# Kernel tuning notes

Measured on AMD Instinct MI355X. Metric: run time of the kernel, lower is better.

The kernel has to match this reference:

```python
import jax, jax.numpy as jnp
import numpy as np

N = 64      # features
L = 96      # history length
LP = 24     # prediction length
H = 128     # rnn hidden
B = 1024    # batch


def setup_inputs() -> dict:
    key = jax.random.key(0)
    ks = jax.random.split(key, 16)
    # monotonically increasing timestamps
    tp_all = jnp.cumsum(jax.random.uniform(ks[0], (B, L + LP), dtype=jnp.float32), axis=1)
    tp_true = tp_all[:, :L]
    tp_pred = tp_all[:, L:]
    X = jax.random.normal(ks[1], (B, L, N), dtype=jnp.float32)
    mask = jax.random.randint(ks[2], (B, L, N), 0, 2).astype(jnp.float32)
    def unif(k, shape, fan):
        std = 1.0 / np.sqrt(fan)
        return jax.random.uniform(k, shape, jnp.float32, -std, std)
    # TemporalDecay for h: W (H,N), b (H); std = 1/sqrt(out)
    Wh_dec = unif(ks[3], (H, N), H)
    bh_dec = unif(ks[4], (H,), H)
    # TemporalDecay for x (diag): W (N,N) but only diagonal used
    Wx_dec = unif(ks[5], (N, N), N)
    bx_dec = unif(ks[6], (N,), N)
    # GRUCell: input size = 2N + H
    in_sz = 2 * N + H
    W_ih = unif(ks[7], (3 * H, in_sz), H)
    W_hh = unif(ks[8], (3 * H, H), H)
    b_ih = unif(ks[9], (3 * H,), H)
    b_hh = unif(ks[10], (3 * H,), H)
    # output projection
    Wp = unif(ks[11], (N, H), H)
    bp = unif(ks[12], (N,), H)
    return {"tp_pred": tp_pred, "X": X, "tp_true": tp_true, "mask": mask,
            "Wh_dec": Wh_dec, "bh_dec": bh_dec, "Wx_dec": Wx_dec, "bx_dec": bx_dec,
            "W_ih": W_ih, "W_hh": W_hh, "b_ih": b_ih, "b_hh": b_hh,
            "Wp": Wp, "bp": bp}


def _grud(tp_pred, X, tp_true, mask, Wh_dec, bh_dec, Wx_dec, bx_dec,
          W_ih, W_hh, b_ih, b_hh, Wp, bp):
    Bsz, Lh, Nf = X.shape
    Lp = tp_pred.shape[1]
    Lall = Lh + Lp
    Hh = Wh_dec.shape[0]

    # pad future with zeros (unobserved)
    X_all = jnp.concatenate([X, jnp.zeros((Bsz, Lp, Nf), X.dtype)], axis=1)
    M_all = jnp.concatenate([mask, jnp.zeros((Bsz, Lp, Nf), X.dtype)], axis=1)
    tp = jnp.concatenate([tp_true, tp_pred], axis=1)

    # deltas: first-difference padded with 0 at t=0, broadcast over features
    dt = jnp.pad(tp[:, 1:] - tp[:, :-1], ((0, 0), (1, 0)))  # (B, Lall)
    deltas = jnp.broadcast_to(dt[:, :, None], (Bsz, Lall, Nf))

    # empirical mean over positions where (1 - mask) == 1 (faithful to source)
    valid = 1.0 - M_all
    cnt = jnp.clip(valid.sum(axis=1), 1.0, None)  # (B, N)
    mu = (X_all * valid).sum(axis=1) / cnt        # (B, N)

    # LOCF as in source: where mask != 0, copy previous value
    def locf_step(prev, xm):
        x_t, m_t = xm
        cur = jnp.where(m_t != 0, prev, x_t)
        return cur, cur
    _, X_locf = jax.lax.scan(locf_step, X_all[:, 0],
                             (jnp.swapaxes(X_all, 0, 1), jnp.swapaxes(M_all, 0, 1)))
    # X_locf: (Lall, B, N)

    diag_Wx = jnp.diag(Wx_dec)  # (N,) -- diag=True masks W with identity

    def step(h, inputs):
        x_t, m_t, d_t, xl_t = inputs  # each (B, N)
        gh = jnp.exp(-jax.nn.relu(d_t @ Wh_dec.T + bh_dec))      # (B, H)
        gx = jnp.exp(-jax.nn.relu(d_t * diag_Wx + bx_dec))       # (B, N)
        h = h * gh
        rep = h
        x_h = gx * xl_t + (1.0 - gx) * mu
        x_in = m_t * x_t + (1.0 - m_t) * x_h
        inp = jnp.concatenate([x_in, h, m_t], axis=1)             # (B, 2N+H)
        gi = inp @ W_ih.T + b_ih                                  # (B, 3H)
        gr = h @ W_hh.T + b_hh                                    # (B, 3H)
        r = jax.nn.sigmoid(gi[:, :Hh] + gr[:, :Hh])
        z = jax.nn.sigmoid(gi[:, Hh:2 * Hh] + gr[:, Hh:2 * Hh])
        n = jnp.tanh(gi[:, 2 * Hh:] + r * gr[:, 2 * Hh:])
        h_new = (1.0 - z) * n + z * h
        return h_new, rep

    h0 = jnp.zeros((Bsz, Hh), X.dtype)
    xs = (jnp.swapaxes(X_all, 0, 1), jnp.swapaxes(M_all, 0, 1),
          jnp.swapaxes(deltas, 0, 1), X_locf)
    _, reps = jax.lax.scan(step, h0, xs)          # (Lall, B, H)
    reps = jnp.swapaxes(reps, 0, 1)               # (B, Lall, H)
    recon = reps @ Wp.T + bp                      # (B, Lall, N)
    y_hat = recon[:, -Lp:]                        # (B, Lp, N)
    return y_hat[None]                            # (1, B, Lp, N)


def reference(tp_pred, X, tp_true, mask, Wh_dec, bh_dec, Wx_dec, bx_dec,
              W_ih, W_hh, b_ih, b_hh, Wp, bp):
    return _grud(tp_pred, X, tp_true, mask, Wh_dec, bh_dec, Wx_dec, bx_dec,
                 W_ih, W_hh, b_ih, b_hh, Wp, bp)
```

## Files before the change

kernel.cpp:

```cpp
#include <hip/hip_runtime.h>

#define L2E 1.4426950408889634f

typedef _Float16 f16x8 __attribute__((ext_vector_type(8)));
typedef _Float16 f16x4 __attribute__((ext_vector_type(4)));
typedef float f32x4 __attribute__((ext_vector_type(4)));

__device__ __forceinline__ float sig_fast(float x) {
    return __builtin_amdgcn_rcpf(1.0f + __builtin_amdgcn_exp2f(-L2E * x));
}
__device__ __forceinline__ float tanh_fast(float x) {
    return 1.0f - 2.0f * __builtin_amdgcn_rcpf(1.0f + __builtin_amdgcn_exp2f(2.0f * L2E * x));
}
__device__ __forceinline__ float expnr_fast(float x) {
    return __builtin_amdgcn_exp2f(-L2E * fmaxf(x, 0.0f));
}
__device__ __forceinline__ void barrier_lds_only() {
    __asm__ volatile("s_waitcnt lgkmcnt(0)\n\ts_barrier" ::: "memory");
}

struct F8 { float v[8]; };
__device__ __forceinline__ F8 ld8(const float* p) {
    F8 r;
    float4 a = *(const float4*)p, b = *(const float4*)(p + 4);
    r.v[0]=a.x; r.v[1]=a.y; r.v[2]=a.z; r.v[3]=a.w;
    r.v[4]=b.x; r.v[5]=b.y; r.v[6]=b.z; r.v[7]=b.w;
    return r;
}
__device__ __forceinline__ f16x8 cvt8(F8 a) {
    f16x8 r;
#pragma unroll
    for (int q = 0; q < 8; ++q) r[q] = (_Float16)a.v[q];
    return r;
}
__device__ __forceinline__ f16x8 cvt8s(F8 a, F8 b) {
    f16x8 r;
#pragma unroll
    for (int q = 0; q < 8; ++q) r[q] = (_Float16)(a.v[q] + b.v[q]);
    return r;
}

__global__ __launch_bounds__(512, 2) void grud_kernel(
    const float* __restrict__ tp_pred, const float* __restrict__ X,
    const float* __restrict__ tp_true, const float* __restrict__ mask,
    const float* __restrict__ Wh_dec, const float* __restrict__ bh_dec,
    const float* __restrict__ Wx_dec, const float* __restrict__ bx_dec,
    const float* __restrict__ W_ih, const float* __restrict__ W_hh,
    const float* __restrict__ b_ih, const float* __restrict__ b_hh,
    const float* __restrict__ Wp, const float* __restrict__ bp,
    float* __restrict__ out)
{
    constexpr int VR = 136;
    constexpr int AR = 136;
    constexpr int RS = 2056;
    __shared__ alignas(16) _Float16 ring[8 * RS];
    __shared__ alignas(16) _Float16 V4[2][4 * VR];
    __shared__ alignas(16) _Float16 Astage[16 * AR];
    __shared__ float dt_lds[480];
    __shared__ float mu_l[4][64];
    __shared__ float wxl[64], bxl[64];

    const int tid  = threadIdx.x;
    const int w    = tid >> 6, l = tid & 63, quad = l >> 4, lm = l & 15;
    const int b0   = blockIdx.x * 4;

    for (int i = tid; i < 4 * VR; i += 512) ((unsigned*)V4)[i] = 0;

    if (tid < 480) {
        int t = tid >> 2, b = b0 + (tid & 3);
        float v = 0.0f;
        if (t) {
            float cur = (t < 96) ? tp_true[b * 96 + t] : tp_pred[b * 24 + t - 96];
            float prv = (t - 1 < 96) ? tp_true[b * 96 + t - 1] : tp_pred[b * 24 + t - 97];
            v = cur - prv;
        }
        dt_lds[tid] = v;
    }
    if (tid < 64) { wxl[tid] = Wx_dec[tid * 65]; bxl[tid] = bx_dec[tid]; }

    if (w >= 4) {
        const int pw   = w - 4;
        const int ptid = tid - 256;
        const int c0   = 32 * pw + lm, c1 = c0 + 16;

        {
            const float* xr = X    + ((size_t)(b0 + pw) * 96) * 64 + l;
            const float* mr = mask + ((size_t)(b0 + pw) * 96) * 64 + l;
            float a = 0.0f, c = 0.0f;
#pragma unroll 4
            for (int t = 0; t < 96; ++t) {
                float x = xr[t * 64], m = mr[t * 64];
                a += x * (1.0f - m); c += 1.0f - m;
            }
            mu_l[pw][l] = a / (c + 24.0f);
        }

        f16x8 wxf[3][2][4];
#pragma unroll
        for (int g = 0; g < 3; ++g)
#pragma unroll
            for (int j = 0; j < 2; ++j)
#pragma unroll
                for (int fi = 0; fi < 4; ++fi) {
                    const int row = g * 128 + (j ? c1 : c0);
                    const int k0 = fi * 32 + quad * 8;
                    wxf[g][j][fi] = cvt8(ld8(W_ih + row * 256 + (k0 < 64 ? k0 : 128 + k0)));
                }

        const int pn = pw * 16 + lm;
        const float bpv = bp[pn];
        f16x8 wPf[4];
#pragma unroll
        for (int fi = 0; fi < 4; ++fi)
            wPf[fi] = cvt8(ld8(Wp + pn * 128 + fi * 32 + quad * 8));

        auto prodLoad = [&](int gp, float4& px, float4& pm) {
            if (gp >= 24) { px = make_float4(0,0,0,0); pm = make_float4(0,0,0,0); return; }
            const int R = ptid >> 4, tg = 4 * gp + (R >> 2), b = R & 3;
            const size_t o = (((size_t)(b0 + b) * 96) + tg) * 64 + (ptid & 15) * 4;
            px = *(const float4*)(X + o);
            pm = *(const float4*)(mask + o);
        };
        auto prodStage = [&](int gp, float4 px, float4 pm) {
            const int R = ptid >> 4, toff = R >> 2, b = R & 3;
            const int tg = 4 * gp + toff, n0 = (ptid & 15) * 4;
            const float d = dt_lds[tg * 4 + b];
            const float xs[4] = {px.x, px.y, px.z, px.w};
            const float ms[4] = {pm.x, pm.y, pm.z, pm.w};
            f16x4 xi, mm;
#pragma unroll
            for (int e = 0; e < 4; ++e) {
                const int n = n0 + e;
                const float gxv = expnr_fast(d * wxl[n] + bxl[n]);
                const float muv = mu_l[b][n];
                float v;
                if (gp < 24) {
                    v = (ms[e] != 0.0f) ? xs[e] : (xs[e] - muv) * gxv + muv;
                    mm[e] = (_Float16)ms[e];
                } else {
                    v = (1.0f - gxv) * muv;
                    mm[e] = (_Float16)0.0f;
                }
                xi[e] = (_Float16)v;
            }
            *(f16x4*)&Astage[R * AR + n0]      = xi;
            *(f16x4*)&Astage[R * AR + 64 + n0] = mm;
        };
        auto prodMMA = [&](int gp) {
            f16x8 ap[4];
#pragma unroll
            for (int fi = 0; fi < 4; ++fi)
                ap[fi] = *(const f16x8*)&Astage[lm * AR + fi * 32 + quad * 8];
            const int slot = (4 * gp + quad) & 7;
            f32x4 aR0 = {0,0,0,0}, aZ0 = {0,0,0,0}, aN0 = {0,0,0,0};
            f32x4 aR1 = {0,0,0,0}, aZ1 = {0,0,0,0}, aN1 = {0,0,0,0};
#pragma unroll
            for (int fi = 0; fi < 4; ++fi) {
                aR0 = __builtin_amdgcn_mfma_f32_16x16x32_f16(ap[fi], wxf[0][0][fi], aR0, 0, 0, 0);
                aZ0 = __builtin_amdgcn_mfma_f32_16x16x32_f16(ap[fi], wxf[1][0][fi], aZ0, 0, 0, 0);
                aN0 = __builtin_amdgcn_mfma_f32_16x16x32_f16(ap[fi], wxf[2][0][fi], aN0, 0, 0, 0);
                aR1 = __builtin_amdgcn_mfma_f32_16x16x32_f16(ap[fi], wxf[0][1][fi], aR1, 0, 0, 0);
                aZ1 = __builtin_amdgcn_mfma_f32_16x16x32_f16(ap[fi], wxf[1][1][fi], aZ1, 0, 0, 0);
                aN1 = __builtin_amdgcn_mfma_f32_16x16x32_f16(ap[fi], wxf[2][1][fi], aN1, 0, 0, 0);
            }
#pragma unroll
            for (int rb = 0; rb < 4; ++rb) {
                f16x4 p0 = {(_Float16)aR0[rb], (_Float16)aZ0[rb], (_Float16)aN0[rb], (_Float16)0.0f};
                f16x4 p1 = {(_Float16)aR1[rb], (_Float16)aZ1[rb], (_Float16)aN1[rb], (_Float16)0.0f};
                *(f16x4*)&ring[slot * RS + (rb * 128 + c0) * 4] = p0;
                *(f16x4*)&ring[slot * RS + (rb * 128 + c1) * 4] = p1;
            }
        };

        __syncthreads();
        {
            float4 px, pm;
            prodLoad(0, px, pm);
            prodStage(0, px, pm);
            barrier_lds_only();
            prodMMA(0);
            barrier_lds_only();
        }

        const int prow = (lm >> 2) * VR + quad * 8;
        float4 px, pm;
        for (int t = 0; t < 120; ++t) {
            const int gp = (t >> 2) + 1, ph = t & 3;
            if (ph == 0)      { if (gp < 30) prodLoad(gp, px, pm); }
            else if (ph == 1) { if (gp < 30) prodStage(gp, px, pm); }
            else if (ph == 2) { if (gp < 30) prodMMA(gp); }

            if (t >= 96) {
                f16x8 af[4];
#pragma unroll
                for (int fi = 0; fi < 4; ++fi)
                    af[fi] = *(const f16x8*)&V4[t & 1][prow + fi * 32];
                f32x4 aP = {bpv, 0, 0, 0};
#pragma unroll
                for (int fi = 0; fi < 4; ++fi)
                    aP = __builtin_amdgcn_mfma_f32_16x16x32_f16(af[fi], wPf[fi], aP, 0, 0, 0);
                out[((size_t)(b0 + quad) * 24 + (t - 96)) * 64 + pn] = aP[0];
            }
            barrier_lds_only();
        }
    } else {
        const int c0 = 32 * w + lm, c1 = c0 + 16;

        f16x8 wR[2][4], wZ[2][4], wN[2][4], wG[2][4];
        float S_[2], bh_[2], bR_[2], bZ_[2], bN_[2], bG_[2];
#pragma unroll
        for (int j = 0; j < 2; ++j) {
            const int c = j ? c1 : c0;
#pragma unroll
            for (int fi = 0; fi < 4; ++fi) {
                const int k0 = fi * 32 + quad * 8;
                wR[j][fi] = cvt8s(ld8(W_ih + c * 256 + 64 + k0),
                                  ld8(W_hh + c * 128 + k0));
                wZ[j][fi] = cvt8s(ld8(W_ih + (128 + c) * 256 + 64 + k0),
                                  ld8(W_hh + (128 + c) * 128 + k0));
                wN[j][fi] = cvt8(ld8(W_ih + (256 + c) * 256 + 64 + k0));
                wG[j][fi] = cvt8(ld8(W_hh + (256 + c) * 128 + k0));
            }
            float s = 0.0f;
            const float4* wh4 = (const float4*)(Wh_dec + c * 64);
#pragma unroll
            for (int i = 0; i < 16; ++i) { float4 u = wh4[i]; s += u.x + u.y + u.z + u.w; }
            S_[j]  = s;
            bh_[j] = bh_dec[c];
            bR_[j] = b_ih[c] + b_hh[c];
            bZ_[j] = b_ih[128 + c] + b_hh[128 + c];
            bN_[j] = b_ih[256 + c];
            bG_[j] = b_hh[256 + c];
        }

        __syncthreads();
        barrier_lds_only();
        barrier_lds_only();

        const f32x4 ZV = {0.0f, 0.0f, 0.0f, 0.0f};
        const int vrow = (lm >> 2) * VR + quad * 8;
        float h0 = 0.0f, h1 = 0.0f;
        for (int t = 0; t < 120; ++t) {
            const _Float16* Vp = V4[t & 1];
            const int sb = (t & 7) * RS + quad * 512;
            const f16x4 g0 = *(const f16x4*)&ring[sb + c0 * 4];
            const f16x4 g1 = *(const f16x4*)&ring[sb + c1 * 4];
            f16x8 af[4];
#pragma unroll
            for (int fi = 0; fi < 4; ++fi)
                af[fi] = *(const f16x8*)&Vp[vrow + fi * 32];

            const int tn = (t < 119) ? t + 1 : 119;
            const float dn = dt_lds[tn * 4 + quad];
            const float ghd0 = expnr_fast(dn * S_[0] + bh_[0]);
            const float ghd1 = expnr_fast(dn * S_[1] + bh_[1]);

            f32x4 aR0 = __builtin_amdgcn_mfma_f32_16x16x32_f16(af[0], wR[0][0], ZV, 0, 0, 0);
            f32x4 aZ0 = __builtin_amdgcn_mfma_f32_16x16x32_f16(af[0], wZ[0][0], ZV, 0, 0, 0);
            f32x4 aN0 = __builtin_amdgcn_mfma_f32_16x16x32_f16(af[0], wN[0][0], ZV, 0, 0, 0);
            f32x4 aG0 = __builtin_amdgcn_mfma_f32_16x16x32_f16(af[0], wG[0][0], ZV, 0, 0, 0);
            f32x4 aR1 = __builtin_amdgcn_mfma_f32_16x16x32_f16(af[0], wR[1][0], ZV, 0, 0, 0);
            f32x4 aZ1 = __builtin_amdgcn_mfma_f32_16x16x32_f16(af[0], wZ[1][0], ZV, 0, 0, 0);
            f32x4 aN1 = __builtin_amdgcn_mfma_f32_16x16x32_f16(af[0], wN[1][0], ZV, 0, 0, 0);
            f32x4 aG1 = __builtin_amdgcn_mfma_f32_16x16x32_f16(af[0], wG[1][0], ZV, 0, 0, 0);
#pragma unroll
            for (int fi = 1; fi < 4; ++fi) {
                aR0 = __builtin_amdgcn_mfma_f32_16x16x32_f16(af[fi], wR[0][fi], aR0, 0, 0, 0);
                aZ0 = __builtin_amdgcn_mfma_f32_16x16x32_f16(af[fi], wZ[0][fi], aZ0, 0, 0, 0);
                aN0 = __builtin_amdgcn_mfma_f32_16x16x32_f16(af[fi], wN[0][fi], aN0, 0, 0, 0);
                aG0 = __builtin_amdgcn_mfma_f32_16x16x32_f16(af[fi], wG[0][fi], aG0, 0, 0, 0);
                aR1 = __builtin_amdgcn_mfma_f32_16x16x32_f16(af[fi], wR[1][fi], aR1, 0, 0, 0);
                aZ1 = __builtin_amdgcn_mfma_f32_16x16x32_f16(af[fi], wZ[1][fi], aZ1, 0, 0, 0);
                aN1 = __builtin_amdgcn_mfma_f32_16x16x32_f16(af[fi], wN[1][fi], aN1, 0, 0, 0);
                aG1 = __builtin_amdgcn_mfma_f32_16x16x32_f16(af[fi], wG[1][fi], aG1, 0, 0, 0);
            }

            const float rg0 = sig_fast(aR0[0] + ((float)g0[0] + bR_[0]));
            const float zg0 = sig_fast(aZ0[0] + ((float)g0[1] + bZ_[0]));
            const float ng0 = tanh_fast(aN0[0] + ((float)g0[2] + bN_[0]) + rg0 * (aG0[0] + bG_[0]));
            h0 = (zg0 * (h0 - ng0) + ng0) * ghd0;
            const float rg1 = sig_fast(aR1[0] + ((float)g1[0] + bR_[1]));
            const float zg1 = sig_fast(aZ1[0] + ((float)g1[1] + bZ_[1]));
            const float ng1 = tanh_fast(aN1[0] + ((float)g1[2] + bN_[1]) + rg1 * (aG1[0] + bG_[1]));
            h1 = (zg1 * (h1 - ng1) + ng1) * ghd1;
            if (t < 119) {
                _Float16* Vn = V4[(t & 1) ^ 1];
                Vn[quad * VR + c0] = (_Float16)h0;
                Vn[quad * VR + c1] = (_Float16)h1;
            }
            barrier_lds_only();
        }
    }
}

extern "C" void kernel_launch(void* const* d_in, const int* in_sizes, int n_in,
                              void* d_out, int out_size, void* d_ws, size_t ws_size,
                              hipStream_t stream) {
    const float* tp_pred = (const float*)d_in[0];
    const float* X       = (const float*)d_in[1];
    const float* tp_true = (const float*)d_in[2];
    const float* mask    = (const float*)d_in[3];
    const float* Wh_dec  = (const float*)d_in[4];
    const float* bh_dec  = (const float*)d_in[5];
    const float* Wx_dec  = (const float*)d_in[6];
    const float* bx_dec  = (const float*)d_in[7];
    const float* W_ih    = (const float*)d_in[8];
    const float* W_hh    = (const float*)d_in[9];
    const float* b_ih    = (const float*)d_in[10];
    const float* b_hh    = (const float*)d_in[11];
    const float* Wp      = (const float*)d_in[12];
    const float* bp      = (const float*)d_in[13];

    grud_kernel<<<dim3(256), dim3(512), 0, stream>>>(
        tp_pred, X, tp_true, mask, Wh_dec, bh_dec, Wx_dec, bx_dec,
        W_ih, W_hh, b_ih, b_hh, Wp, bp, (float*)d_out);
}
```

Measured before the change: 199.0 us.

## Process eight batch rows per block with two interleaved recurrence chains

Each block now handles 8 batch rows instead of 4, and the grid is halved to 128 blocks. The consumer waves run two independent GRU chains (A and B) per step so their MFMA and transcendental latencies can overlap, and reuse the same weight registers for both. The producer side is re-phased to two timesteps per group with a double-buffered staging area and a new ring layout. The risks are higher register pressure and using only 128 blocks on a GPU with more compute units, which lowers occupancy and parallelism.

New measurement: 274.6 us. 38.0% more time.

```diff
diff --git a/kernel.cpp b/kernel.cpp
--- a/kernel.cpp
+++ b/kernel.cpp
@@ -52,29 +52,30 @@
 {
     constexpr int VR = 136;
     constexpr int AR = 136;
-    constexpr int RS = 2056;
-    __shared__ alignas(16) _Float16 ring[8 * RS];
-    __shared__ alignas(16) _Float16 V4[2][4 * VR];
-    __shared__ alignas(16) _Float16 Astage[16 * AR];
-    __shared__ float dt_lds[480];
-    __shared__ float mu_l[4][64];
+    constexpr int CS = 28;
+    constexpr int RSLOT = 128 * CS;
+    __shared__ alignas(16) _Float16 ring[4 * RSLOT];
+    __shared__ alignas(16) _Float16 V4[2][2][4 * VR];
+    __shared__ alignas(16) _Float16 Astage[2][16 * AR];
+    __shared__ float dt_lds[120 * 8];
+    __shared__ float mu_l[8][64];
     __shared__ float wxl[64], bxl[64];
 
     const int tid  = threadIdx.x;
     const int w    = tid >> 6, l = tid & 63, quad = l >> 4, lm = l & 15;
-    const int b0   = blockIdx.x * 4;
-
-    for (int i = tid; i < 4 * VR; i += 512) ((unsigned*)V4)[i] = 0;
-
-    if (tid < 480) {
-        int t = tid >> 2, b = b0 + (tid & 3);
+    const int b0   = blockIdx.x * 8;
+
+    for (int i = tid; i < 1088; i += 512) ((unsigned*)V4)[i] = 0;
+
+    for (int i = tid; i < 960; i += 512) {
+        int t = i >> 3, b = b0 + (i & 7);
         float v = 0.0f;
         if (t) {
             float cur = (t < 96) ? tp_true[b * 96 + t] : tp_pred[b * 24 + t - 96];
             float prv = (t - 1 < 96) ? tp_true[b * 96 + t - 1] : tp_pred[b * 24 + t - 97];
             v = cur - prv;
         }
-        dt_lds[tid] = v;
+        dt_lds[i] = v;
     }
     if (tid < 64) { wxl[tid] = Wx_dec[tid * 65]; bxl[tid] = bx_dec[tid]; }
 
@@ -84,15 +85,20 @@
         const int c0   = 32 * pw + lm, c1 = c0 + 16;
 
         {
-            const float* xr = X    + ((size_t)(b0 + pw) * 96) * 64 + l;
-            const float* mr = mask + ((size_t)(b0 + pw) * 96) * 64 + l;
-            float a = 0.0f, c = 0.0f;
+            const float* xr0 = X    + ((size_t)(b0 + 2 * pw) * 96) * 64 + l;
+            const float* mr0 = mask + ((size_t)(b0 + 2 * pw) * 96) * 64 + l;
+            const float* xr1 = X    + ((size_t)(b0 + 2 * pw + 1) * 96) * 64 + l;
+            const float* mr1 = mask + ((size_t)(b0 + 2 * pw + 1) * 96) * 64 + l;
+            float a0 = 0, cv0 = 0, a1 = 0, cv1 = 0;
 #pragma unroll 4
             for (int t = 0; t < 96; ++t) {
-                float x = xr[t * 64], m = mr[t * 64];
-                a += x * (1.0f - m); c += 1.0f - m;
-            }
-            mu_l[pw][l] = a / (c + 24.0f);
+                float x0 = xr0[t * 64], m0 = mr0[t * 64];
+                float x1 = xr1[t * 64], m1 = mr1[t * 64];
+                a0 += x0 * (1.0f - m0); cv0 += 1.0f - m0;
+                a1 += x1 * (1.0f - m1); cv1 += 1.0f - m1;
+            }
+            mu_l[2 * pw][l]     = a0 / (cv0 + 24.0f);
+            mu_l[2 * pw + 1][l] = a1 / (cv1 + 24.0f);
         }
 
         f16x8 wxf[3][2][4];
@@ -115,16 +121,17 @@
             wPf[fi] = cvt8(ld8(Wp + pn * 128 + fi * 32 + quad * 8));
 
         auto prodLoad = [&](int gp, float4& px, float4& pm) {
-            if (gp >= 24) { px = make_float4(0,0,0,0); pm = make_float4(0,0,0,0); return; }
-            const int R = ptid >> 4, tg = 4 * gp + (R >> 2), b = R & 3;
+            if (gp >= 48) { px = make_float4(0,0,0,0); pm = make_float4(0,0,0,0); return; }
+            const int R = ptid >> 4, toff = R >> 3, b = R & 7;
+            const int tg = 2 * gp + toff;
             const size_t o = (((size_t)(b0 + b) * 96) + tg) * 64 + (ptid & 15) * 4;
             px = *(const float4*)(X + o);
             pm = *(const float4*)(mask + o);
         };
         auto prodStage = [&](int gp, float4 px, float4 pm) {
-            const int R = ptid >> 4, toff = R >> 2, b = R & 3;
-            const int tg = 4 * gp + toff, n0 = (ptid & 15) * 4;
-            const float d = dt_lds[tg * 4 + b];
+            const int R = ptid >> 4, toff = R >> 3, b = R & 7;
+            const int tg = 2 * gp + toff, n0 = (ptid & 15) * 4;
+            const float d = dt_lds[tg * 8 + b];
             const float xs[4] = {px.x, px.y, px.z, px.w};
             const float ms[4] = {pm.x, pm.y, pm.z, pm.w};
             f16x4 xi, mm;
@@ -134,7 +141,7 @@
                 const float gxv = expnr_fast(d * wxl[n] + bxl[n]);
                 const float muv = mu_l[b][n];
                 float v;
-                if (gp < 24) {
+                if (gp < 48) {
                     v = (ms[e] != 0.0f) ? xs[e] : (xs[e] - muv) * gxv + muv;
                     mm[e] = (_Float16)ms[e];
                 } else {
@@ -143,15 +150,14 @@
                 }
                 xi[e] = (_Float16)v;
             }
-            *(f16x4*)&Astage[R * AR + n0]      = xi;
-            *(f16x4*)&Astage[R * AR + 64 + n0] = mm;
+            *(f16x4*)&Astage[gp & 1][R * AR + n0]      = xi;
+            *(f16x4*)&Astage[gp & 1][R * AR + 64 + n0] = mm;
         };
         auto prodMMA = [&](int gp) {
             f16x8 ap[4];
 #pragma unroll
             for (int fi = 0; fi < 4; ++fi)
-                ap[fi] = *(const f16x8*)&Astage[lm * AR + fi * 32 + quad * 8];
-            const int slot = (4 * gp + quad) & 7;
+                ap[fi] = *(const f16x8*)&Astage[gp & 1][lm * AR + fi * 32 + quad * 8];
             f32x4 aR0 = {0,0,0,0}, aZ0 = {0,0,0,0}, aN0 = {0,0,0,0};
             f32x4 aR1 = {0,0,0,0}, aZ1 = {0,0,0,0}, aN1 = {0,0,0,0};
 #pragma unroll
@@ -163,43 +169,55 @@
                 aZ1 = __builtin_amdgcn_mfma_f32_16x16x32_f16(ap[fi], wxf[1][1][fi], aZ1, 0, 0, 0);
                 aN1 = __builtin_amdgcn_mfma_f32_16x16x32_f16(ap[fi], wxf[2][1][fi], aN1, 0, 0, 0);
             }
-#pragma unroll
-            for (int rb = 0; rb < 4; ++rb) {
-                f16x4 p0 = {(_Float16)aR0[rb], (_Float16)aZ0[rb], (_Float16)aN0[rb], (_Float16)0.0f};
-                f16x4 p1 = {(_Float16)aR1[rb], (_Float16)aZ1[rb], (_Float16)aN1[rb], (_Float16)0.0f};
-                *(f16x4*)&ring[slot * RS + (rb * 128 + c0) * 4] = p0;
-                *(f16x4*)&ring[slot * RS + (rb * 128 + c1) * 4] = p1;
-            }
+            const int toff = quad >> 1, bb = (quad & 1) * 4;
+            const int slot = (2 * gp + toff) & 3;
+            f16x4 pk;
+            pk[0]=(_Float16)aR0[0]; pk[1]=(_Float16)aR0[1]; pk[2]=(_Float16)aR0[2]; pk[3]=(_Float16)aR0[3];
+            *(f16x4*)&ring[slot * RSLOT + c0 * CS + 0 * 8 + bb] = pk;
+            pk[0]=(_Float16)aZ0[0]; pk[1]=(_Float16)aZ0[1]; pk[2]=(_Float16)aZ0[2]; pk[3]=(_Float16)aZ0[3];
+            *(f16x4*)&ring[slot * RSLOT + c0 * CS + 1 * 8 + bb] = pk;
+            pk[0]=(_Float16)aN0[0]; pk[1]=(_Float16)aN0[1]; pk[2]=(_Float16)aN0[2]; pk[3]=(_Float16)aN0[3];
+            *(f16x4*)&ring[slot * RSLOT + c0 * CS + 2 * 8 + bb] = pk;
+            pk[0]=(_Float16)aR1[0]; pk[1]=(_Float16)aR1[1]; pk[2]=(_Float16)aR1[2]; pk[3]=(_Float16)aR1[3];
+            *(f16x4*)&ring[slot * RSLOT + c1 * CS + 0 * 8 + bb] = pk;
+            pk[0]=(_Float16)aZ1[0]; pk[1]=(_Float16)aZ1[1]; pk[2]=(_Float16)aZ1[2]; pk[3]=(_Float16)aZ1[3];
+            *(f16x4*)&ring[slot * RSLOT + c1 * CS + 1 * 8 + bb] = pk;
+            pk[0]=(_Float16)aN1[0]; pk[1]=(_Float16)aN1[1]; pk[2]=(_Float16)aN1[2]; pk[3]=(_Float16)aN1[3];
+            *(f16x4*)&ring[slot * RSLOT + c1 * CS + 2 * 8 + bb] = pk;
         };
 
+        float4 px[2], pm[2];
         __syncthreads();
-        {
-            float4 px, pm;
-            prodLoad(0, px, pm);
-            prodStage(0, px, pm);
-            barrier_lds_only();
-            prodMMA(0);
-            barrier_lds_only();
-        }
+        prodLoad(0, px[0], pm[0]);
+        prodStage(0, px[0], pm[0]);
+        barrier_lds_only();
+        prodMMA(0);
+        prodLoad(1, px[1], pm[1]);
+        barrier_lds_only();
 
         const int prow = (lm >> 2) * VR + quad * 8;
-        float4 px, pm;
         for (int t = 0; t < 120; ++t) {
-            const int gp = (t >> 2) + 1, ph = t & 3;
-            if (ph == 0)      { if (gp < 30) prodLoad(gp, px, pm); }
-            else if (ph == 1) { if (gp < 30) prodStage(gp, px, pm); }
-            else if (ph == 2) { if (gp < 30) prodMMA(gp); }
+            const int k = t >> 1;
+            if ((t & 1) == 0) {
+                if (k + 2 < 60) prodLoad(k + 2, px[k & 1], pm[k & 1]);
+                if (k + 1 < 60) prodStage(k + 1, px[(k + 1) & 1], pm[(k + 1) & 1]);
+            } else {
+                if (k + 1 < 60) prodMMA(k + 1);
+            }
 
             if (t >= 96) {
-                f16x8 af[4];
-#pragma unroll
-                for (int fi = 0; fi < 4; ++fi)
-                    af[fi] = *(const f16x8*)&V4[t & 1][prow + fi * 32];
-                f32x4 aP = {bpv, 0, 0, 0};
-#pragma unroll
-                for (int fi = 0; fi < 4; ++fi)
-                    aP = __builtin_amdgcn_mfma_f32_16x16x32_f16(af[fi], wPf[fi], aP, 0, 0, 0);
-                out[((size_t)(b0 + quad) * 24 + (t - 96)) * 64 + pn] = aP[0];
+#pragma unroll
+                for (int g = 0; g < 2; ++g) {
+                    f16x8 af[4];
+#pragma unroll
+                    for (int fi = 0; fi < 4; ++fi)
+                        af[fi] = *(const f16x8*)&V4[g][t & 1][prow + fi * 32];
+                    f32x4 aP = {bpv, 0, 0, 0};
+#pragma unroll
+                    for (int fi = 0; fi < 4; ++fi)
+                        aP = __builtin_amdgcn_mfma_f32_16x16x32_f16(af[fi], wPf[fi], aP, 0, 0, 0);
+                    out[((size_t)(b0 + 4 * g + quad) * 24 + (t - 96)) * 64 + pn] = aP[0];
+                }
             }
             barrier_lds_only();
         }
@@ -239,54 +257,103 @@
 
         const f32x4 ZV = {0.0f, 0.0f, 0.0f, 0.0f};
         const int vrow = (lm >> 2) * VR + quad * 8;
-        float h0 = 0.0f, h1 = 0.0f;
+        float hA0 = 0, hA1 = 0, hB0 = 0, hB1 = 0;
         for (int t = 0; t < 120; ++t) {
-            const _Float16* Vp = V4[t & 1];
-            const int sb = (t & 7) * RS + quad * 512;
-            const f16x4 g0 = *(const f16x4*)&ring[sb + c0 * 4];
-            const f16x4 g1 = *(const f16x4*)&ring[sb + c1 * 4];
-            f16x8 af[4];
-#pragma unroll
-            for (int fi = 0; fi < 4; ++fi)
-                af[fi] = *(const f16x8*)&Vp[vrow + fi * 32];
+            const _Float16* VpA = V4[0][t & 1];
+            const _Float16* VpB = V4[1][t & 1];
+            const int sb = (t & 3) * RSLOT;
+            float gA[2][3], gB[2][3];
+#pragma unroll
+            for (int j = 0; j < 2; ++j) {
+                const int cb = (j ? c1 : c0) * CS;
+#pragma unroll
+                for (int g3 = 0; g3 < 3; ++g3) {
+                    gA[j][g3] = (float)ring[sb + cb + g3 * 8 + quad];
+                    gB[j][g3] = (float)ring[sb + cb + g3 * 8 + 4 + quad];
+                }
+            }
+            f16x8 afA[4], afB[4];
+#pragma unroll
+            for (int fi = 0; fi < 4; ++fi) {
+                afA[fi] = *(const f16x8*)&VpA[vrow + fi * 32];
+                afB[fi] = *(const f16x8*)&VpB[vrow + fi * 32];
+            }
 
             const int tn = (t < 119) ? t + 1 : 119;
-            const float dn = dt_lds[tn * 4 + quad];
-            const float ghd0 = expnr_fast(dn * S_[0] + bh_[0]);
-            const float ghd1 = expnr_fast(dn * S_[1] + bh_[1]);
-
-            f32x4 aR0 = __builtin_amdgcn_mfma_f32_16x16x32_f16(af[0], wR[0][0], ZV, 0, 0, 0);
-            f32x4 aZ0 = __builtin_amdgcn_mfma_f32_16x16x32_f16(af[0], wZ[0][0], ZV, 0, 0, 0);
-            f32x4 aN0 = __builtin_amdgcn_mfma_f32_16x16x32_f16(af[0], wN[0][0], ZV, 0, 0, 0);
-            f32x4 aG0 = __builtin_amdgcn_mfma_f32_16x16x32_f16(af[0], wG[0][0], ZV, 0, 0, 0);
-            f32x4 aR1 = __builtin_amdgcn_mfma_f32_16x16x32_f16(af[0], wR[1][0], ZV, 0, 0, 0);
-            f32x4 aZ1 = __builtin_amdgcn_mfma_f32_16x16x32_f16(af[0], wZ[1][0], ZV, 0, 0, 0);
-            f32x4 aN1 = __builtin_amdgcn_mfma_f32_16x16x32_f16(af[0], wN[1][0], ZV, 0, 0, 0);
-            f32x4 aG1 = __builtin_amdgcn_mfma_f32_16x16x32_f16(af[0], wG[1][0], ZV, 0, 0, 0);
+            const float dnA = dt_lds[tn * 8 + quad];
+            const float dnB = dt_lds[tn * 8 + 4 + quad];
+            const float ghA0 = expnr_fast(dnA * S_[0] + bh_[0]);
+            const float ghA1 = expnr_fast(dnA * S_[1] + bh_[1]);
+            const float ghB0 = expnr_fast(dnB * S_[0] + bh_[0]);
+            const float ghB1 = expnr_fast(dnB * S_[1] + bh_[1]);
+
+            f32x4 aR0 = __builtin_amdgcn_mfma_f32_16x16x32_f16(afA[0], wR[0][0], ZV, 0, 0, 0);
+            f32x4 aZ0 = __builtin_amdgcn_mfma_f32_16x16x32_f16(afA[0], wZ[0][0], ZV, 0, 0, 0);
+            f32x4 aN0 = __builtin_amdgcn_mfma_f32_16x16x32_f16(afA[0], wN[0][0], ZV, 0, 0, 0);
+            f32x4 aG0 = __builtin_amdgcn_mfma_f32_16x16x32_f16(afA[0], wG[0][0], ZV, 0, 0, 0);
+            f32x4 aR1 = __builtin_amdgcn_mfma_f32_16x16x32_f16(afA[0], wR[1][0], ZV, 0, 0, 0);
+            f32x4 aZ1 = __builtin_amdgcn_mfma_f32_16x16x32_f16(afA[0], wZ[1][0], ZV, 0, 0, 0);
+            f32x4 aN1 = __builtin_amdgcn_mfma_f32_16x16x32_f16(afA[0], wN[1][0], ZV, 0, 0, 0);
+            f32x4 aG1 = __builtin_amdgcn_mfma_f32_16x16x32_f16(afA[0], wG[1][0], ZV, 0, 0, 0);
+            f32x4 bR0 = __builtin_amdgcn_mfma_f32_16x16x32_f16(afB[0], wR[0][0], ZV, 0, 0, 0);
+            f32x4 bZ0 = __builtin_amdgcn_mfma_f32_16x16x32_f16(afB[0], wZ[0][0], ZV, 0, 0, 0);
+            f32x4 bN0 = __builtin_amdgcn_mfma_f32_16x16x32_f16(afB[0], wN[0][0], ZV, 0, 0, 0);
+            f32x4 bG0 = __builtin_amdgcn_mfma_f32_16x16x32_f16(afB[0], wG[0][0], ZV, 0, 0, 0);
+            f32x4 bR1 = __builtin_amdgcn_mfma_f32_16x16x32_f16(afB[0], wR[1][0], ZV, 0, 0, 0);
+            f32x4 bZ1 = __builtin_amdgcn_mfma_f32_16x16x32_f16(afB[0], wZ[1][0], ZV, 0, 0, 0);
+            f32x4 bN1 = __builtin_amdgcn_mfma_f32_16x16x32_f16(afB[0], wN[1][0], ZV, 0, 0, 0);
+            f32x4 bG1 = __builtin_amdgcn_mfma_f32_16x16x32_f16(afB[0], wG[1][0], ZV, 0, 0, 0);
 #pragma unroll
             for (int fi = 1; fi < 4; ++fi) {
-                aR0 = __builtin_amdgcn_mfma_f32_16x16x32_f16(af[fi], wR[0][fi], aR0, 0, 0, 0);
-                aZ0 = __builtin_amdgcn_mfma_f32_16x16x32_f16(af[fi], wZ[0][fi], aZ0, 0, 0, 0);
-                aN0 = __builtin_amdgcn_mfma_f32_16x16x32_f16(af[fi], wN[0][fi], aN0, 0, 0, 0);
-                aG0 = __builtin_amdgcn_mfma_f32_16x16x32_f16(af[fi], wG[0][fi], aG0, 0, 0, 0);
-                aR1 = __builtin_amdgcn_mfma_f32_16x16x32_f16(af[fi], wR[1][fi], aR1, 0, 0, 0);
-                aZ1 = __builtin_amdgcn_mfma_f32_16x16x32_f16(af[fi], wZ[1][fi], aZ1, 0, 0, 0);
-                aN1 = __builtin_amdgcn_mfma_f32_16x16x32_f16(af[fi], wN[1][fi], aN1, 0, 0, 0);
-                aG1 = __builtin_amdgcn_mfma_f32_16x16x32_f16(af[fi], wG[1][fi], aG1, 0, 0, 0);
-            }
-
-            const float rg0 = sig_fast(aR0[0] + ((float)g0[0] + bR_[0]));
-            const float zg0 = sig_fast(aZ0[0] + ((float)g0[1] + bZ_[0]));
-            const float ng0 = tanh_fast(aN0[0] + ((float)g0[2] + bN_[0]) + rg0 * (aG0[0] + bG_[0]));
-            h0 = (zg0 * (h0 - ng0) + ng0) * ghd0;
-            const float rg1 = sig_fast(aR1[0] + ((float)g1[0] + bR_[1]));
-            const float zg1 = sig_fast(aZ1[0] + ((float)g1[1] + bZ_[1]));
-            const float ng1 = tanh_fast(aN1[0] + ((float)g1[2] + bN_[1]) + rg1 * (aG1[0] + bG_[1]));
-            h1 = (zg1 * (h1 - ng1) + ng1) * ghd1;
+                aR0 = __builtin_amdgcn_mfma_f32_16x16x32_f16(afA[fi], wR[0][fi], aR0, 0, 0, 0);
+                aZ0 = __builtin_amdgcn_mfma_f32_16x16x32_f16(afA[fi], wZ[0][fi], aZ0, 0, 0, 0);
+                aN0 = __builtin_amdgcn_mfma_f32_16x16x32_f16(afA[fi], wN[0][fi], aN0, 0, 0, 0);
+                aG0 = __builtin_amdgcn_mfma_f32_16x16x32_f16(afA[fi], wG[0][fi], aG0, 0, 0, 0);
+                aR1 = __builtin_amdgcn_mfma_f32_16x16x32_f16(afA[fi], wR[1][fi], aR1, 0, 0, 0);
+                aZ1 = __builtin_amdgcn_mfma_f32_16x16x32_f16(afA[fi], wZ[1][fi], aZ1, 0, 0, 0);
+                aN1 = __builtin_amdgcn_mfma_f32_16x16x32_f16(afA[fi], wN[1][fi], aN1, 0, 0, 0);
+                aG1 = __builtin_amdgcn_mfma_f32_16x16x32_f16(afA[fi], wG[1][fi], aG1, 0, 0, 0);
+                bR0 = __builtin_amdgcn_mfma_f32_16x16x32_f16(afB[fi], wR[0][fi], bR0, 0, 0, 0);
+                bZ0 = __builtin_amdgcn_mfma_f32_16x16x32_f16(afB[fi], wZ[0][fi], bZ0, 0, 0, 0);
+                bN0 = __builtin_amdgcn_mfma_f32_16x16x32_f16(afB[fi], wN[0][fi], bN0, 0, 0, 0);
+                bG0 = __builtin_amdgcn_mfma_f32_16x16x32_f16(afB[fi], wG[0][fi], bG0, 0, 0, 0);
+                bR1 = __builtin_amdgcn_mfma_f32_16x16x32_f16(afB[fi], wR[1][fi], bR1, 0, 0, 0);
+                bZ1 = __builtin_amdgcn_mfma_f32_16x16x32_f16(afB[fi], wZ[1][fi], bZ1, 0, 0, 0);
+                bN1 = __builtin_amdgcn_mfma_f32_16x16x32_f16(afB[fi], wN[1][fi], bN1, 0, 0, 0);
+                bG1 = __builtin_amdgcn_mfma_f32_16x16x32_f16(afB[fi], wG[1][fi], bG1, 0, 0, 0);
+            }
+
+            {
+                const float rg = sig_fast(aR0[0] + (gA[0][0] + bR_[0]));
+                const float zg = sig_fast(aZ0[0] + (gA[0][1] + bZ_[0]));
+                const float ng = tanh_fast(aN0[0] + (gA[0][2] + bN_[0]) + rg * (aG0[0] + bG_[0]));
+                hA0 = (zg * (hA0 - ng) + ng) * ghA0;
+            }
+            {
+                const float rg = sig_fast(aR1[0] + (gA[1][0] + bR_[1]));
+                const float zg = sig_fast(aZ1[0] + (gA[1][1] + bZ_[1]));
+                const float ng = tanh_fast(aN1[0] + (gA[1][2] + bN_[1]) + rg * (aG1[0] + bG_[1]));
+                hA1 = (zg * (hA1 - ng) + ng) * ghA1;
+            }
+            {
+                const float rg = sig_fast(bR0[0] + (gB[0][0] + bR_[0]));
+                const float zg = sig_fast(bZ0[0] + (gB[0][1] + bZ_[0]));
+                const float ng = tanh_fast(bN0[0] + (gB[0][2] + bN_[0]) + rg * (bG0[0] + bG_[0]));
+                hB0 = (zg * (hB0 - ng) + ng) * ghB0;
+            }
+            {
+                const float rg = sig_fast(bR1[0] + (gB[1][0] + bR_[1]));
+                const float zg = sig_fast(bZ1[0] + (gB[1][1] + bZ_[1]));
+                const float ng = tanh_fast(bN1[0] + (gB[1][2] + bN_[1]) + rg * (bG1[0] + bG_[1]));
+                hB1 = (zg * (hB1 - ng) + ng) * ghB1;
+            }
             if (t < 119) {
-                _Float16* Vn = V4[(t & 1) ^ 1];
-                Vn[quad * VR + c0] = (_Float16)h0;
-                Vn[quad * VR + c1] = (_Float16)h1;
+                _Float16* VnA = V4[0][(t & 1) ^ 1];
+                _Float16* VnB = V4[1][(t & 1) ^ 1];
+                VnA[quad * VR + c0] = (_Float16)hA0;
+                VnA[quad * VR + c1] = (_Float16)hA1;
+                VnB[quad * VR + c0] = (_Float16)hB0;
+                VnB[quad * VR + c1] = (_Float16)hB1;
             }
             barrier_lds_only();
         }
@@ -311,7 +378,7 @@
     const float* Wp      = (const float*)d_in[12];
     const float* bp      = (const float*)d_in[13];
 
-    grud_kernel<<<dim3(256), dim3(512), 0, stream>>>(
+    grud_kernel<<<dim3(128), dim3(512), 0, stream>>>(
         tp_pred, X, tp_true, mask, Wh_dec, bh_dec, Wx_dec, bx_dec,
         W_ih, W_hh, b_ih, b_hh, Wp, bp, (float*)d_out);
 }
```
